# Optimization experiments

Hardware: AMD Instinct MI355X
Metric: run time of the kernel (lower is better)

## Reference

```python
import jax, jax.numpy as jnp
import numpy as np

ALPHA = 0.5      # APPNP teleport prob (AG_EAGCN alpha=0.5)
DEPTH = 3        # APPNP depth
PROP_NUMS = 3    # EAGCN propagation steps


def _adj_process(adj, eps):
    # adj[adj<eps]=0 ; symmetrize ; add I ; D^-1/2 A D^-1/2 (inf->0)
    N = adj.shape[1]
    adj = jnp.where(adj < eps, 0.0, adj)
    adj = 0.5 * (adj + jnp.swapaxes(adj, 1, 2))
    adj = adj + jnp.eye(N, dtype=adj.dtype)
    d = jnp.sum(adj, axis=2)                                   # [n, N]
    dinv = jnp.where(d > 0, 1.0 / jnp.sqrt(jnp.where(d > 0, d, 1.0)), 0.0)
    return adj * dinv[:, :, None] * dinv[:, None, :]


def _eagcn(seg, edge, ws1, bs1, ws11, bs11, ws2, bs2, ws3, bs3, wmlp, bmlp, wgcn, bgcn):
    n, c, h, w = seg.shape
    hw = h * w
    num_s = ws1.shape[0]
    # conv_s1 (1x1)
    seg_s = jnp.einsum('nchw,sc->nshw', seg, ws1) + bs1[None, :, None, None]
    theta_T = seg_s.reshape(n, num_s, hw)       # raw view, as in torch
    theta = seg_s.reshape(n, hw, num_s)         # raw view (NOT transpose)
    # channel attention: diag_channel_att = ca ca^T is rank-1 ->
    # theta @ (ca ca^T) @ theta_T = (theta@ca) outer (ca@theta_T)
    pooled = seg.mean(axis=(2, 3))                              # [n, c]
    ca = jax.nn.relu(pooled @ wmlp.T + bmlp)                    # [n, num_s]
    u = jnp.einsum('nps,ns->np', theta, ca)                     # [n, hw]
    v = jnp.einsum('ns,nsq->nq', ca, theta_T)                   # [n, hw]
    sim_c = _adj_process(u[:, :, None] * v[:, None, :], 0.15)
    # spatial branch
    seg_c = jnp.einsum('nchw,sc->nshw', seg, ws11) + bs11[None, :, None, None]
    sigma = seg_c.reshape(n, num_s, hw)
    sigma_T = seg_c.reshape(n, hw, num_s)
    sigma_out = jnp.einsum('nps,nsq->npq', sigma_T, sigma)      # [n, hw, hw]
    edge_m = seg * edge
    seg_ss = (ws2 * seg.max(axis=1) + bs2).reshape(n, 1, hw)    # 1x1 conv on 1 chan
    edge_mm = (ws3 * edge_m.max(axis=1) + bs3).reshape(n, hw, 1)
    sim_s = _adj_process(sigma_out * (edge_mm * seg_ss), 0.15)
    sim = _adj_process(sim_c + sim_s, 0.0)
    # GCN_layer: relu(conv1d(seg @ sim)) + seg, residual
    seg2 = seg.reshape(n, c, hw)
    seg_sim = jnp.einsum('nck,nkq->ncq', seg2, sim)
    out = jax.nn.relu(jnp.einsum('oc,ncq->noq', wgcn, seg_sim) + bgcn[None, :, None]) + seg2
    return out.reshape(n, c, h, w), sim


def _appnp(seg, adj, wa1, ba1, wa2, ba2):
    n, c, h, w = seg.shape
    x = seg.reshape(n, h * w, c)                                # raw view
    t = jax.nn.relu(jax.nn.relu(x @ wa1.T + ba1) @ wa2.T + ba2)
    out = t
    for _ in range(DEPTH):
        out = (1.0 - ALPHA) * jnp.einsum('npq,nqc->npc', adj, out) + ALPHA * t
    return out


def _forward(seg, edge, ws1, bs1, ws11, bs11, ws2, bs2, ws3, bs3,
             wmlp, bmlp, wgcn, bgcn, wa1, ba1, wa2, ba2):
    ori = seg
    n, c, h, w = seg.shape
    adjs = []
    for _ in range(PROP_NUMS):
        seg, adj = _eagcn(seg, edge, ws1, bs1, ws11, bs11, ws2, bs2, ws3, bs3,
                          wmlp, bmlp, wgcn, bgcn)
        adjs.append(adj)
    adj = (adjs[0] + adjs[1] + adjs[2]) / float(PROP_NUMS)      # mean aggregation
    adj = _adj_process(adj, 0.0)
    # graph regularizer
    dirichlet = jnp.einsum('nii->', adj)                        # sum of traces
    N = adj.shape[1]
    gamma = 0.1; beta = 0.1; alpha_r = 0.1
    rowsum = jnp.sum(adj, axis=2)                               # adj @ ones
    f_A = (-beta * jnp.sum(jnp.log(rowsum), axis=1)[:, None, None] / N
           + gamma * jnp.sqrt(jnp.sum(adj * adj)) / (N ** 2))
    reg = alpha_r * dirichlet + f_A                             # [n,1,1]
    out = _appnp(ori, adj, wa1, ba1, wa2, ba2).reshape(n, c, h, w)
    return out, reg


def setup_inputs() -> dict:
    key = jax.random.key(0)
    ks = jax.random.split(key, 10)
    n, c, h, w = 8, 256, 32, 32
    num_s, hid = 64, 3

    def lin(k, out_f, in_f):
        lim = 1.0 / np.sqrt(in_f)
        return jax.random.uniform(k, (out_f, in_f), jnp.float32, -lim, lim)

    return dict(
        seg=jax.random.normal(ks[0], (n, c, h, w), jnp.float32),
        edge=jax.random.uniform(ks[1], (n, c, h, w), jnp.float32),
        ws1=lin(ks[2], num_s, c), bs1=jnp.zeros((num_s,), jnp.float32),
        ws11=lin(ks[3], num_s, c), bs11=jnp.zeros((num_s,), jnp.float32),
        ws2=jnp.asarray(0.7, jnp.float32), bs2=jnp.asarray(0.1, jnp.float32),
        ws3=jnp.asarray(0.6, jnp.float32), bs3=jnp.asarray(0.1, jnp.float32),
        wmlp=lin(ks[4], num_s, c), bmlp=jnp.zeros((num_s,), jnp.float32),
        wgcn=lin(ks[5], c, c), bgcn=jnp.zeros((c,), jnp.float32),
        wa1=lin(ks[6], hid, c), ba1=jnp.zeros((hid,), jnp.float32),
        wa2=lin(ks[7], c, hid), ba2=jnp.zeros((c,), jnp.float32),
    )


def reference(seg, edge, ws1, bs1, ws11, bs11, ws2, bs2, ws3, bs3,
              wmlp, bmlp, wgcn, bgcn, wa1, ba1, wa2, ba2):
    return _forward(seg, edge, ws1, bs1, ws11, bs11, ws2, bs2, ws3, bs3,
                    wmlp, bmlp, wgcn, bgcn, wa1, ba1, wa2, ba2)
```

## Files before the change

### kernel.cpp

```cpp
#include <hip/hip_runtime.h>
#include <math.h>

#define NB 8
#define C 256
#define HW 1024
#define NS 64

typedef unsigned short u16;
typedef __attribute__((ext_vector_type(8))) short bf16x8;
typedef __attribute__((ext_vector_type(4))) float f32x4;

__device__ __forceinline__ u16 f2bf(float x) {
    union { float f; unsigned u; } v; v.f = x;
    unsigned r = v.u + 0x7fffu + ((v.u >> 16) & 1u);
    return (u16)(r >> 16);
}
__device__ __forceinline__ float bf2f(u16 h) {
    union { unsigned u; float f; } v; v.u = ((unsigned)h) << 16; return v.f;
}
__device__ __forceinline__ void splitbf(float x, u16& h, u16& l) {
    h = f2bf(x);
    l = f2bf(x - bf2f(h));
}

__device__ __forceinline__ float blockReduceSum(float v, float* s4) {
    #pragma unroll
    for (int o = 32; o; o >>= 1) v += __shfl_down(v, o);
    __syncthreads();
    if ((threadIdx.x & 63) == 0) s4[threadIdx.x >> 6] = v;
    __syncthreads();
    return s4[0] + s4[1] + s4[2] + s4[3];
}

__global__ void k_prepw(const float* __restrict__ ws1, const float* __restrict__ bs1,
                        const float* __restrict__ ws11, const float* __restrict__ bs11,
                        float* __restrict__ WCAT, float* __restrict__ BCAT) {
    int tid = blockIdx.x * 256 + threadIdx.x;
    if (tid < 64 * C) {
        WCAT[tid] = ws1[tid];
        WCAT[64 * C + tid] = ws11[tid];
    }
    if (tid < 64) { BCAT[tid] = bs1[tid]; BCAT[64 + tid] = bs11[tid]; }
}

template<int R, int CIN>
__global__ void k_transp(const float* __restrict__ in, long long sIn,
                         float* __restrict__ outp, long long sOut) {
    int ti = blockIdx.x, tj = blockIdx.y, n = blockIdx.z, tid = threadIdx.x;
    int i0 = ti * 64, j0 = tj * 64;
    const float* ib = in + (size_t)n * sIn;
    float* ob = outp + (size_t)n * sOut;
    __shared__ float L[64][65];
    for (int idx = tid; idx < 4096; idx += 256) {
        int r = idx >> 6, c = idx & 63;
        L[r][c] = ib[(size_t)(i0 + r) * CIN + (j0 + c)];
    }
    __syncthreads();
    for (int idx = tid; idx < 4096; idx += 256) {
        int r = idx >> 6, c = idx & 63;
        ob[(size_t)(j0 + r) * R + (i0 + c)] = L[c][r];
    }
}

__global__ void k_pooled(const float* __restrict__ seg, float* __restrict__ pooled) {
    int c = blockIdx.x, n = blockIdx.y, tid = threadIdx.x;
    const float* row = seg + ((size_t)n * C + c) * HW;
    float acc = row[tid] + row[tid + 256] + row[tid + 512] + row[tid + 768];
    __shared__ float s4[4];
    float r = blockReduceSum(acc, s4);
    if (tid == 0) pooled[n * C + c] = r * (1.0f / HW);
}

__global__ void k_ca(const float* __restrict__ pooled, const float* __restrict__ wmlp,
                     const float* __restrict__ bmlp, float* __restrict__ ca) {
    int n = blockIdx.x, s = threadIdx.x;
    __shared__ float pl[C];
    for (int i = s; i < C; i += 64) pl[i] = pooled[n * C + i];
    __syncthreads();
    float acc = 0.f;
    for (int c = 0; c < C; ++c) acc += pl[c] * wmlp[s * C + c];
    float r = acc + bmlp[s];
    ca[n * NS + s] = r > 0.f ? r : 0.f;
}

__global__ void k_maxes(const float* __restrict__ seg, const float* __restrict__ edge,
                        float* __restrict__ smax, float* __restrict__ emax) {
    int pos = blockIdx.x * 256 + threadIdx.x;
    int n = blockIdx.y, ch = blockIdx.z;
    const float* sb = seg + (size_t)n * C * HW + (size_t)(ch * 32) * HW + pos;
    const float* eb = edge + (size_t)n * C * HW + (size_t)(ch * 32) * HW + pos;
    float ms = -3.402823466e38f, me = -3.402823466e38f;
    #pragma unroll 8
    for (int c = 0; c < 32; ++c) {
        float s = sb[(size_t)c * HW];
        ms = fmaxf(ms, s);
        me = fmaxf(me, s * eb[(size_t)c * HW]);
    }
    smax[((size_t)ch * NB + n) * HW + pos] = ms;
    emax[((size_t)ch * NB + n) * HW + pos] = me;
}

__global__ void k_maxfin(const float* __restrict__ smax, const float* __restrict__ emax,
                         const float* __restrict__ ws2, const float* __restrict__ bs2,
                         const float* __restrict__ ws3, const float* __restrict__ bs3,
                         float* __restrict__ segss, float* __restrict__ edgemm) {
    int pos = blockIdx.x * 256 + threadIdx.x;
    int n = blockIdx.y;
    float ms = -3.402823466e38f, me = -3.402823466e38f;
    #pragma unroll
    for (int ch = 0; ch < 8; ++ch) {
        ms = fmaxf(ms, smax[((size_t)ch * NB + n) * HW + pos]);
        me = fmaxf(me, emax[((size_t)ch * NB + n) * HW + pos]);
    }
    segss[n * HW + pos] = ws2[0] * ms + bs2[0];
    edgemm[n * HW + pos] = ws3[0] * me + bs3[0];
}

__global__ void k_uv(const float* __restrict__ segsc, const float* __restrict__ ca,
                     float* __restrict__ u, float* __restrict__ vv) {
    int pos = blockIdx.x * 256 + threadIdx.x;
    int n = blockIdx.y, role = blockIdx.z;
    const float* flat = segsc + (size_t)n * 128 * HW;
    __shared__ float cs[NS];
    if (threadIdx.x < NS) cs[threadIdx.x] = ca[n * NS + threadIdx.x];
    __syncthreads();
    if (role == 0) {
        const float* base = flat + (size_t)pos * NS;
        float acc = 0.f;
        #pragma unroll
        for (int s = 0; s < NS; ++s) acc += base[s] * cs[s];
        u[n * HW + pos] = acc;
    } else {
        float acc = 0.f;
        #pragma unroll
        for (int s = 0; s < NS; ++s) acc += cs[s] * flat[(size_t)s * HW + pos];
        vv[n * HW + pos] = acc;
    }
}

__global__ __launch_bounds__(256) void k_bbuild(
    const float* __restrict__ Aflat, long long sA,
    const float* __restrict__ CT,
    const float* __restrict__ em, const float* __restrict__ ss,
    float* __restrict__ B, float* __restrict__ dsum) {
    constexpr int LDK = 72;
    constexpr int TSZ = 64 * LDK;
    __shared__ __align__(16) u16 sm[4 * 2 * TSZ];
    int pi = blockIdx.x, n = blockIdx.y, tid = threadIdx.x;
    int i = 0, base = 0;
    while (pi >= base + (16 - i)) { base += 16 - i; ++i; }
    int j = i + (pi - base);
    int i0 = i * 64, j0 = j * 64;
    bool diag = (i == j);
    const float* An = Aflat + (size_t)n * sA;
    const float* Cn = CT + (size_t)n * NS * HW;
    const float* emn = em + n * HW;
    const float* ssn = ss + n * HW;
    float* Bn = B + (size_t)n * HW * HW;

    auto stage = [&](int t, const float* src, int r0) {
        u16* hi = sm + t * 2 * TSZ;
        u16* lo = hi + TSZ;
        #pragma unroll
        for (int p = 0; p < 2; ++p) {
            int e = (p * 256 + tid) * 8;
            int r = e >> 6, k0 = e & 63;
            const float* s = src + (size_t)(r0 + r) * 64 + k0;
            float4 w0 = *(const float4*)s;
            float4 w1 = *(const float4*)(s + 4);
            float xs[8] = {w0.x, w0.y, w0.z, w0.w, w1.x, w1.y, w1.z, w1.w};
            u16 h[8], l[8];
            #pragma unroll
            for (int q = 0; q < 8; ++q) splitbf(xs[q], h[q], l[q]);
            int b = r * LDK + k0;
            *(bf16x8*)(hi + b) = (bf16x8){(short)h[0], (short)h[1], (short)h[2], (short)h[3],
                                          (short)h[4], (short)h[5], (short)h[6], (short)h[7]};
            *(bf16x8*)(lo + b) = (bf16x8){(short)l[0], (short)l[1], (short)l[2], (short)l[3],
                                          (short)l[4], (short)l[5], (short)l[6], (short)l[7]};
        }
    };
    stage(0, An, i0);
    stage(2, Cn, i0);
    if (!diag) { stage(1, An, j0); stage(3, Cn, j0); }
    __syncthreads();

    int lane = tid & 63, wv = tid >> 6;
    int g = lane >> 4;
    f32x4 acc1[4], acc2[4];
    #pragma unroll
    for (int ni = 0; ni < 4; ++ni) {
        acc1[ni] = (f32x4){0.f, 0.f, 0.f, 0.f};
        acc2[ni] = (f32x4){0.f, 0.f, 0.f, 0.f};
    }

    const u16* AiH = sm + 0 * 2 * TSZ; const u16* AiL = AiH + TSZ;
    const u16* AjH = sm + 1 * 2 * TSZ; const u16* AjL = AjH + TSZ;
    const u16* BiH = sm + 2 * 2 * TSZ; const u16* BiL = BiH + TSZ;
    const u16* BjH = sm + 3 * 2 * TSZ; const u16* BjL = BjH + TSZ;

    #pragma unroll
    for (int kk = 0; kk < 2; ++kk) {
        int kl = kk * 32 + g * 8;
        int arow = wv * 16 + (lane & 15);
        bf16x8 a1h = *(const bf16x8*)(AiH + arow * LDK + kl);
        bf16x8 a1l = *(const bf16x8*)(AiL + arow * LDK + kl);
        bf16x8 a2h, a2l;
        if (!diag) {
            a2h = *(const bf16x8*)(AjH + arow * LDK + kl);
            a2l = *(const bf16x8*)(AjL + arow * LDK + kl);
        }
        #pragma unroll
        for (int ni = 0; ni < 4; ++ni) {
            int brow = ni * 16 + (lane & 15);
            if (diag) {
                bf16x8 bh = *(const bf16x8*)(BiH + brow * LDK + kl);
                bf16x8 bl = *(const bf16x8*)(BiL + brow * LDK + kl);
                acc1[ni] = __builtin_amdgcn_mfma_f32_16x16x32_bf16(a1h, bh, acc1[ni], 0, 0, 0);
                acc1[ni] = __builtin_amdgcn_mfma_f32_16x16x32_bf16(a1h, bl, acc1[ni], 0, 0, 0);
                acc1[ni] = __builtin_amdgcn_mfma_f32_16x16x32_bf16(a1l, bh, acc1[ni], 0, 0, 0);
            } else {
                bf16x8 b1h = *(const bf16x8*)(BjH + brow * LDK + kl);
                bf16x8 b1l = *(const bf16x8*)(BjL + brow * LDK + kl);
                acc1[ni] = __builtin_amdgcn_mfma_f32_16x16x32_bf16(a1h, b1h, acc1[ni], 0, 0, 0);
                acc1[ni] = __builtin_amdgcn_mfma_f32_16x16x32_bf16(a1h, b1l, acc1[ni], 0, 0, 0);
                acc1[ni] = __builtin_amdgcn_mfma_f32_16x16x32_bf16(a1l, b1h, acc1[ni], 0, 0, 0);
                bf16x8 b2h = *(const bf16x8*)(BiH + brow * LDK + kl);
                bf16x8 b2l = *(const bf16x8*)(BiL + brow * LDK + kl);
                acc2[ni] = __builtin_amdgcn_mfma_f32_16x16x32_bf16(a2h, b2h, acc2[ni], 0, 0, 0);
                acc2[ni] = __builtin_amdgcn_mfma_f32_16x16x32_bf16(a2h, b2l, acc2[ni], 0, 0, 0);
                acc2[ni] = __builtin_amdgcn_mfma_f32_16x16x32_bf16(a2l, b2h, acc2[ni], 0, 0, 0);
            }
        }
    }
    __syncthreads();

    float* t1 = (float*)sm;
    float* t2 = t1 + 64 * 65;
    float x[4][4], y[4][4];
    #pragma unroll
    for (int ni = 0; ni < 4; ++ni) {
        int col = ni * 16 + (lane & 15);
        #pragma unroll
        for (int r = 0; r < 4; ++r) {
            int row = wv * 16 + g * 4 + r;
            float v1 = acc1[ni][r] * emn[i0 + row] * ssn[j0 + col];
            v1 = v1 < 0.15f ? 0.f : v1;
            x[ni][r] = v1;
            t1[row * 65 + col] = v1;
            if (!diag) {
                float v2 = acc2[ni][r] * emn[j0 + row] * ssn[i0 + col];
                v2 = v2 < 0.15f ? 0.f : v2;
                y[ni][r] = v2;
                t2[row * 65 + col] = v2;
            }
        }
    }
    __syncthreads();

    float rs1[4] = {0.f, 0.f, 0.f, 0.f}, rs2[4] = {0.f, 0.f, 0.f, 0.f};
    #pragma unroll
    for (int ni = 0; ni < 4; ++ni) {
        int col = ni * 16 + (lane & 15);
        #pragma unroll
        for (int r = 0; r < 4; ++r) {
            int row = wv * 16 + g * 4 + r;
            float s1 = 0.5f * (x[ni][r] + (diag ? t1[col * 65 + row] : t2[col * 65 + row]));
            Bn[(size_t)(i0 + row) * HW + j0 + col] = s1;
            rs1[r] += s1;
            if (!diag) {
                float s2 = 0.5f * (y[ni][r] + t1[col * 65 + row]);
                Bn[(size_t)(j0 + row) * HW + i0 + col] = s2;
                rs2[r] += s2;
            }
        }
    }
    #pragma unroll
    for (int r = 0; r < 4; ++r) {
        #pragma unroll
        for (int m = 1; m < 16; m <<= 1) {
            rs1[r] += __shfl_xor(rs1[r], m);
            rs2[r] += __shfl_xor(rs2[r], m);
        }
    }
    if ((lane & 15) == 0) {
        #pragma unroll
        for (int r = 0; r < 4; ++r) {
            int row = wv * 16 + g * 4 + r;
            atomicAdd(&dsum[n * HW + i0 + row], rs1[r]);
            if (!diag) atomicAdd(&dsum[n * HW + j0 + row], rs2[r]);
        }
    }
}

template<int BM, int BN, int MODE>
__global__ __launch_bounds__(256) void k_mfma2(
    const float* __restrict__ Af, long long sA, int lda,
    const float* __restrict__ Bf, long long sB, int ldb,
    int K,
    float* __restrict__ Cf, long long sCf, int ldc,
    const float* __restrict__ e1,
    const float* __restrict__ e2, long long se2) {
    constexpr int WM = BM / 32;
    constexpr int WN = BN / 32;
    constexpr int LDK = 72;
    __shared__ __align__(16) u16 sAH[BM * LDK], sAL[BM * LDK];
    __shared__ __align__(16) u16 sBH[BN * LDK], sBL[BN * LDK];
    int n = blockIdx.z;
    int q0 = blockIdx.x * BN, m0 = blockIdx.y * BM;
    int tid = threadIdx.x, lane = tid & 63, wv = tid >> 6;
    int wm = wv >> 1, wn = wv & 1;

    f32x4 acc[WM][WN];
    #pragma unroll
    for (int mi = 0; mi < WM; ++mi)
        #pragma unroll
        for (int ni = 0; ni < WN; ++ni)
            acc[mi][ni] = (f32x4){0.f, 0.f, 0.f, 0.f};

    for (int kt = 0; kt < K; kt += 64) {
        #pragma unroll
        for (int p = 0; p < BM / 32; ++p) {
            int e = (p * 256 + tid) * 8;
            int r = e >> 6, k0 = e & 63;
            const float* src = Af + (size_t)n * sA + (size_t)(m0 + r) * lda + kt + k0;
            float4 w0 = *(const float4*)src;
            float4 w1 = *(const float4*)(src + 4);
            float xs[8] = {w0.x, w0.y, w0.z, w0.w, w1.x, w1.y, w1.z, w1.w};
            u16 h[8], l[8];
            #pragma unroll
            for (int q = 0; q < 8; ++q) splitbf(xs[q], h[q], l[q]);
            int b = r * LDK + k0;
            *(bf16x8*)(sAH + b) = (bf16x8){(short)h[0], (short)h[1], (short)h[2], (short)h[3],
                                           (short)h[4], (short)h[5], (short)h[6], (short)h[7]};
            *(bf16x8*)(sAL + b) = (bf16x8){(short)l[0], (short)l[1], (short)l[2], (short)l[3],
                                           (short)l[4], (short)l[5], (short)l[6], (short)l[7]};
        }
        #pragma unroll
        for (int p = 0; p < BN / 32; ++p) {
            int e = (p * 256 + tid) * 8;
            int c = e >> 6, k0 = e & 63;
            const float* src = Bf + (size_t)n * sB + (size_t)(q0 + c) * ldb + kt + k0;
            float4 w0 = *(const float4*)src;
            float4 w1 = *(const float4*)(src + 4);
            float xs[8] = {w0.x, w0.y, w0.z, w0.w, w1.x, w1.y, w1.z, w1.w};
            u16 h[8], l[8];
            #pragma unroll
            for (int q = 0; q < 8; ++q) splitbf(xs[q], h[q], l[q]);
            int b = c * LDK + k0;
            *(bf16x8*)(sBH + b) = (bf16x8){(short)h[0], (short)h[1], (short)h[2], (short)h[3],
                                           (short)h[4], (short)h[5], (short)h[6], (short)h[7]};
            *(bf16x8*)(sBL + b) = (bf16x8){(short)l[0], (short)l[1], (short)l[2], (short)l[3],
                                           (short)l[4], (short)l[5], (short)l[6], (short)l[7]};
        }
        __syncthreads();
        #pragma unroll
        for (int kk = 0; kk < 2; ++kk) {
            int klocal = kk * 32 + (lane >> 4) * 8;
            bf16x8 aH[WM], aL[WM], bH[WN], bL[WN];
            #pragma unroll
            for (int mi = 0; mi < WM; ++mi) {
                int row = (wm * WM + mi) * 16 + (lane & 15);
                aH[mi] = *(const bf16x8*)(sAH + row * LDK + klocal);
                aL[mi] = *(const bf16x8*)(sAL + row * LDK + klocal);
            }
            #pragma unroll
            for (int ni = 0; ni < WN; ++ni) {
                int col = (wn * WN + ni) * 16 + (lane & 15);
                bH[ni] = *(const bf16x8*)(sBH + col * LDK + klocal);
                bL[ni] = *(const bf16x8*)(sBL + col * LDK + klocal);
            }
            #pragma unroll
            for (int mi = 0; mi < WM; ++mi)
                #pragma unroll
                for (int ni = 0; ni < WN; ++ni) {
                    acc[mi][ni] = __builtin_amdgcn_mfma_f32_16x16x32_bf16(aH[mi], bH[ni], acc[mi][ni], 0, 0, 0);
                    acc[mi][ni] = __builtin_amdgcn_mfma_f32_16x16x32_bf16(aH[mi], bL[ni], acc[mi][ni], 0, 0, 0);
                    acc[mi][ni] = __builtin_amdgcn_mfma_f32_16x16x32_bf16(aL[mi], bH[ni], acc[mi][ni], 0, 0, 0);
                }
        }
        __syncthreads();
    }

    #pragma unroll
    for (int mi = 0; mi < WM; ++mi) {
        #pragma unroll
        for (int ni = 0; ni < WN; ++ni) {
            int col = q0 + (wn * WN + ni) * 16 + (lane & 15);
            int rowb = m0 + (wm * WM + mi) * 16 + (lane >> 4) * 4;
            #pragma unroll
            for (int r = 0; r < 4; ++r) {
                int row = rowb + r;
                float val = acc[mi][ni][r];
                if (MODE == 0) {
                    Cf[(size_t)n * sCf + (size_t)col * ldc + row] = val;
                } else if (MODE == 2) {
                    val = fmaxf(val + e1[row], 0.f) + e2[(size_t)n * se2 + (size_t)row * ldc + col];
                    Cf[(size_t)n * sCf + (size_t)row * ldc + col] = val;
                } else if (MODE == 3) {
                    val = 0.5f * val + 0.5f * e2[(size_t)n * se2 + (size_t)row * ldc + col];
                    Cf[(size_t)n * sCf + (size_t)row * ldc + col] = val;
                } else if (MODE == 4) {
                    val = 0.5f * val + 0.5f * e2[(size_t)n * se2 + (size_t)row * HW + col];
                    Cf[(size_t)n * sCf + (size_t)col * ldc + row] = val;
                } else {
                    val = val + e1[row];
                    Cf[(size_t)n * sCf + (size_t)row * ldc + col] = val;
                }
            }
        }
    }
}

__global__ void k_dinv(const float* __restrict__ u, const float* __restrict__ vv,
                       const float* __restrict__ dsum,
                       float* __restrict__ dcinv, float* __restrict__ dsinv) {
    int p = blockIdx.x, n = blockIdx.y, tid = threadIdx.x;
    const float* un = u + n * HW;
    const float* vn = vv + n * HW;
    float up = un[p], vp = vn[p];
    float acc_c = 0.f;
    for (int q = tid; q < HW; q += 256) {
        float x = up * vn[q]; x = x < 0.15f ? 0.f : x;
        float y = un[q] * vp; y = y < 0.15f ? 0.f : y;
        acc_c += 0.5f * (x + y);
    }
    __shared__ float s4[4];
    acc_c = blockReduceSum(acc_c, s4);
    if (tid == 0) {
        dcinv[n * HW + p] = 1.0f / sqrtf(acc_c + 1.0f);
        dsinv[n * HW + p] = 1.0f / sqrtf(dsum[n * HW + p] + 1.0f);
    }
}

__global__ void k_simsum(const float* __restrict__ B, const float* __restrict__ u,
                         const float* __restrict__ vv, const float* __restrict__ dcinv,
                         const float* __restrict__ dsinv, float* __restrict__ dfinv) {
    int p = blockIdx.x, n = blockIdx.y, tid = threadIdx.x;
    const float* Bb = B + (size_t)n * HW * HW + (size_t)p * HW;
    const float* un = u + n * HW;
    const float* vn = vv + n * HW;
    const float* dci = dcinv + n * HW;
    const float* dsi = dsinv + n * HW;
    float up = un[p], vp = vn[p], dcp = dci[p], dsp = dsi[p];
    float acc = 0.f;
    for (int q = tid; q < HW; q += 256) {
        float x = up * vn[q]; x = x < 0.15f ? 0.f : x;
        float y = un[q] * vp; y = y < 0.15f ? 0.f : y;
        float delta = (q == p) ? 1.0f : 0.0f;
        float val = (0.5f * (x + y) + delta) * dcp * dci[q] + (Bb[q] + delta) * dsp * dsi[q];
        acc += val;
    }
    __shared__ float s4[4];
    acc = blockReduceSum(acc, s4);
    if (tid == 0) dfinv[n * HW + p] = 1.0f / sqrtf(acc + 1.0f);
}

__global__ void k_norm_accum(float* __restrict__ B, const float* __restrict__ u,
                             const float* __restrict__ vv, const float* __restrict__ dcinv,
                             const float* __restrict__ dsinv, const float* __restrict__ dfinv,
                             float* __restrict__ ACC, int first) {
    int p = blockIdx.x, n = blockIdx.y, tid = threadIdx.x;
    float* Bb = B + (size_t)n * HW * HW + (size_t)p * HW;
    float* Ab = ACC + (size_t)n * HW * HW + (size_t)p * HW;
    const float* un = u + n * HW;
    const float* vn = vv + n * HW;
    const float* dci = dcinv + n * HW;
    const float* dsi = dsinv + n * HW;
    const float* df = dfinv + n * HW;
    float up = un[p], vp = vn[p], dcp = dci[p], dsp = dsi[p], dfp = df[p];
    for (int q = tid; q < HW; q += 256) {
        float x = up * vn[q]; x = x < 0.15f ? 0.f : x;
        float y = un[q] * vp; y = y < 0.15f ? 0.f : y;
        float delta = (q == p) ? 1.0f : 0.0f;
        float sim_pre = (0.5f * (x + y) + delta) * dcp * dci[q] + (Bb[q] + delta) * dsp * dsi[q];
        float val = (sim_pre + delta) * dfp * df[q];
        Bb[q] = val;
        Ab[q] = first ? val : (Ab[q] + val);
    }
}

__global__ void k_final_rowsum(const float* __restrict__ ACC, float* __restrict__ dinv) {
    int p = blockIdx.x, n = blockIdx.y, tid = threadIdx.x;
    const float* Ab = ACC + (size_t)n * HW * HW + (size_t)p * HW;
    float acc = 0.f;
    for (int q = tid; q < HW; q += 256) acc += Ab[q];
    __shared__ float s4[4];
    acc = blockReduceSum(acc, s4);
    if (tid == 0) dinv[n * HW + p] = 1.0f / sqrtf(acc * (1.0f / 3.0f) + 1.0f);
}

__global__ void k_final_norm(float* __restrict__ ACC, const float* __restrict__ dinv,
                             float* __restrict__ rowsf, float* __restrict__ diagrow,
                             float* __restrict__ sqrow) {
    int p = blockIdx.x, n = blockIdx.y, tid = threadIdx.x;
    float* Ab = ACC + (size_t)n * HW * HW + (size_t)p * HW;
    const float* di = dinv + n * HW;
    float dp = di[p];
    float accr = 0.f, accsq = 0.f, accd = 0.f;
    for (int q = tid; q < HW; q += 256) {
        float val = (Ab[q] * (1.0f / 3.0f) + ((q == p) ? 1.f : 0.f)) * dp * di[q];
        Ab[q] = val;
        accr += val;
        accsq += val * val;
        if (q == p) accd = val;
    }
    __shared__ float s4[4];
    accr = blockReduceSum(accr, s4);
    accsq = blockReduceSum(accsq, s4);
    accd = blockReduceSum(accd, s4);
    if (tid == 0) {
        rowsf[n * HW + p] = accr;
        sqrow[n * HW + p] = accsq;
        diagrow[n * HW + p] = accd;
    }
}

__global__ void k_scal(const float* __restrict__ diagrow, const float* __restrict__ sqrow,
                       float* __restrict__ scal) {
    int tid = threadIdx.x;
    float a = 0.f, b = 0.f;
    for (int i = tid; i < NB * HW; i += 256) { a += diagrow[i]; b += sqrow[i]; }
    __shared__ float s4[4];
    a = blockReduceSum(a, s4);
    b = blockReduceSum(b, s4);
    if (tid == 0) { scal[0] = a; scal[1] = b; }
}

__global__ void k_reg(const float* __restrict__ rowsf, const float* __restrict__ scal,
                      float* __restrict__ outreg) {
    int n = blockIdx.x, tid = threadIdx.x;
    float acc = 0.f;
    for (int p = tid; p < HW; p += 256) acc += logf(rowsf[n * HW + p]);
    __shared__ float s4[4];
    acc = blockReduceSum(acc, s4);
    if (tid == 0) {
        float f = -0.1f * acc / 1024.0f + 0.1f * sqrtf(scal[1]) / 1048576.0f;
        outreg[n] = 0.1f * scal[0] + f;
    }
}

__global__ void k_appnp_t(const float* __restrict__ ori, const float* __restrict__ wa1,
                          const float* __restrict__ ba1, const float* __restrict__ wa2,
                          const float* __restrict__ ba2, float* __restrict__ T) {
    int p = blockIdx.x, n = blockIdx.y, tid = threadIdx.x;
    const float* x = ori + (size_t)n * C * HW + (size_t)p * C;
    float xv = x[tid];
    __shared__ float s4[4];
    __shared__ float h[3];
    float d0 = blockReduceSum(xv * wa1[0 * C + tid], s4);
    float d1 = blockReduceSum(xv * wa1[1 * C + tid], s4);
    float d2 = blockReduceSum(xv * wa1[2 * C + tid], s4);
    if (tid == 0) {
        h[0] = fmaxf(d0 + ba1[0], 0.f);
        h[1] = fmaxf(d1 + ba1[1], 0.f);
        h[2] = fmaxf(d2 + ba1[2], 0.f);
    }
    __syncthreads();
    float t = h[0] * wa2[tid * 3 + 0] + h[1] * wa2[tid * 3 + 1] + h[2] * wa2[tid * 3 + 2] + ba2[tid];
    T[(size_t)n * HW * C + (size_t)p * C + tid] = fmaxf(t, 0.f);
}

extern "C" void kernel_launch(void* const* d_in, const int* in_sizes, int n_in,
                              void* d_out, int out_size, void* d_ws, size_t ws_size,
                              hipStream_t stream) {
    const float* seg_in = (const float*)d_in[0];
    const float* edge   = (const float*)d_in[1];
    const float* ws1    = (const float*)d_in[2];
    const float* bs1    = (const float*)d_in[3];
    const float* ws11   = (const float*)d_in[4];
    const float* bs11   = (const float*)d_in[5];
    const float* ws2    = (const float*)d_in[6];
    const float* bs2    = (const float*)d_in[7];
    const float* ws3    = (const float*)d_in[8];
    const float* bs3    = (const float*)d_in[9];
    const float* wmlp   = (const float*)d_in[10];
    const float* bmlp   = (const float*)d_in[11];
    const float* wgcn   = (const float*)d_in[12];
    const float* bgcn   = (const float*)d_in[13];
    const float* wa1    = (const float*)d_in[14];
    const float* ba1    = (const float*)d_in[15];
    const float* wa2    = (const float*)d_in[16];
    const float* ba2    = (const float*)d_in[17];

    float* out = (float*)d_out;
    float* w = (float*)d_ws;
    float* SEG_A   = w; w += (size_t)NB * C * HW;
    float* SEG_SIMT= w; w += (size_t)NB * C * HW;
    float* SEGSC   = w; w += (size_t)NB * 128 * HW;
    float* SEGCT   = w; w += (size_t)NB * NS * HW;
    float* SEGT    = w; w += (size_t)NB * HW * C;
    float* TBUF    = w; w += (size_t)NB * HW * C;
    float* OBUF    = w; w += (size_t)NB * HW * C;
    float* BBUF    = w; w += (size_t)NB * HW * HW;
    float* ACCUM   = w; w += (size_t)NB * HW * HW;
    float* MAXS    = w; w += (size_t)8 * NB * HW;
    float* MAXE    = w; w += (size_t)8 * NB * HW;
    float* WCAT    = w; w += (size_t)128 * C;
    float* BCAT    = w; w += 128;
    float* ubuf    = w; w += NB * HW;
    float* vbuf    = w; w += NB * HW;
    float* ssbuf   = w; w += NB * HW;
    float* embuf   = w; w += NB * HW;
    float* dsum    = w; w += NB * HW;
    float* dcinv   = w; w += NB * HW;
    float* dsinv   = w; w += NB * HW;
    float* dfinv   = w; w += NB * HW;
    float* rowsf   = w; w += NB * HW;
    float* diagrow = w; w += NB * HW;
    float* sqrow   = w; w += NB * HW;
    float* pooled  = w; w += NB * C;
    float* cabuf   = w; w += NB * NS;
    float* scal    = w; w += 16;

    const long long sAdj = (long long)HW * HW;
    const long long sSeg = (long long)C * HW;
    const long long sSC  = (long long)128 * HW;

    k_prepw<<<dim3(64), 256, 0, stream>>>(ws1, bs1, ws11, bs11, WCAT, BCAT);

    for (int it = 0; it < 3; ++it) {
        const float* seg_src = (it == 0) ? seg_in : SEG_A;
        k_transp<C, HW><<<dim3(4, 16, NB), 256, 0, stream>>>(seg_src, sSeg, SEGT, sSeg);
        k_mfma2<64, 64, 5><<<dim3(16, 2, NB), 256, 0, stream>>>(
            WCAT, 0, C, SEGT, sSeg, C, C,
            SEGSC, sSC, HW, BCAT, nullptr, 0);
        k_transp<NS, HW><<<dim3(1, 16, NB), 256, 0, stream>>>(SEGSC + (size_t)64 * HW, sSC, SEGCT, (long long)NS * HW);
        k_pooled<<<dim3(C, NB), 256, 0, stream>>>(seg_src, pooled);
        k_ca<<<dim3(NB), 64, 0, stream>>>(pooled, wmlp, bmlp, cabuf);
        k_maxes<<<dim3(4, NB, 8), 256, 0, stream>>>(seg_src, edge, MAXS, MAXE);
        k_maxfin<<<dim3(4, NB), 256, 0, stream>>>(MAXS, MAXE, ws2, bs2, ws3, bs3, ssbuf, embuf);
        k_uv<<<dim3(4, NB, 2), 256, 0, stream>>>(SEGSC, cabuf, ubuf, vbuf);
        hipMemsetAsync(dsum, 0, (size_t)NB * HW * sizeof(float), stream);
        k_bbuild<<<dim3(136, NB), 256, 0, stream>>>(SEGSC + (size_t)64 * HW, sSC, SEGCT,
                                                    embuf, ssbuf, BBUF, dsum);
        k_dinv<<<dim3(HW, NB), 256, 0, stream>>>(ubuf, vbuf, dsum, dcinv, dsinv);
        k_simsum<<<dim3(HW, NB), 256, 0, stream>>>(BBUF, ubuf, vbuf, dcinv, dsinv, dfinv);
        k_norm_accum<<<dim3(HW, NB), 256, 0, stream>>>(BBUF, ubuf, vbuf, dcinv, dsinv, dfinv,
                                                       ACCUM, it == 0 ? 1 : 0);
        k_mfma2<64, 64, 0><<<dim3(16, 4, NB), 256, 0, stream>>>(
            seg_src, sSeg, HW, BBUF, sAdj, HW, HW,
            SEG_SIMT, sSeg, C, nullptr, nullptr, 0);
        k_mfma2<64, 64, 2><<<dim3(16, 4, NB), 256, 0, stream>>>(
            wgcn, 0, C, SEG_SIMT, sSeg, C, C,
            SEG_A, sSeg, HW, bgcn, seg_src, sSeg);
    }

    k_final_rowsum<<<dim3(HW, NB), 256, 0, stream>>>(ACCUM, dcinv);
    k_final_norm<<<dim3(HW, NB), 256, 0, stream>>>(ACCUM, dcinv, rowsf, diagrow, sqrow);
    k_scal<<<dim3(1), 256, 0, stream>>>(diagrow, sqrow, scal);
    k_reg<<<dim3(NB), 256, 0, stream>>>(rowsf, scal, out + (size_t)NB * C * HW);

    k_appnp_t<<<dim3(HW, NB), 256, 0, stream>>>(seg_in, wa1, ba1, wa2, ba2, TBUF);
    k_transp<HW, C><<<dim3(16, 4, NB), 256, 0, stream>>>(TBUF, sSeg, SEG_SIMT, sSeg);
    k_mfma2<64, 64, 3><<<dim3(16, 4, NB), 256, 0, stream>>>(
        SEG_SIMT, sSeg, HW, ACCUM, sAdj, HW, HW,
        TBUF, sSeg, HW, nullptr, SEG_SIMT, sSeg);
    k_mfma2<64, 64, 3><<<dim3(16, 4, NB), 256, 0, stream>>>(
        TBUF, sSeg, HW, ACCUM, sAdj, HW, HW,
        OBUF, sSeg, HW, nullptr, SEG_SIMT, sSeg);
    k_mfma2<64, 64, 4><<<dim3(16, 4, NB), 256, 0, stream>>>(
        OBUF, sSeg, HW, ACCUM, sAdj, HW, HW,
        out, sSeg, C, nullptr, SEG_SIMT, sSeg);
}
```

Baseline: 701.4 us.

## Store operands pre-split into bf16 hi/lo planes instead of splitting in GEMM loads

Producers now write every GEMM operand as separate bf16 hi and lo arrays: transposes, epilogues, the normalization kernels and the weights. The MFMA and bbuild kernels then copy bf16x8 vectors straight into shared memory without per-element float splitting. This removes the repeated split work inside the GEMM tile loops. Operand reads drop from 4 to 4 bytes total (hi+lo), so traffic is the same, but the large HW×HW matrices are re-read many times. It adds extra write traffic wherever both fp32 and split copies are kept, and it grows the workspace.

```diff
diff --git a/kernel.cpp b/kernel.cpp
--- a/kernel.cpp
+++ b/kernel.cpp
@@ -32,24 +32,33 @@
     return s4[0] + s4[1] + s4[2] + s4[3];
 }
 
+__global__ void k_presplit(const float* __restrict__ in, u16* __restrict__ oh,
+                           u16* __restrict__ ol, int nElem) {
+    for (int i = blockIdx.x * 256 + threadIdx.x; i < nElem; i += gridDim.x * 256) {
+        u16 h, l; splitbf(in[i], h, l);
+        oh[i] = h; ol[i] = l;
+    }
+}
+
 __global__ void k_prepw(const float* __restrict__ ws1, const float* __restrict__ bs1,
                         const float* __restrict__ ws11, const float* __restrict__ bs11,
-                        float* __restrict__ WCAT, float* __restrict__ BCAT) {
+                        u16* __restrict__ WCH, u16* __restrict__ WCL, float* __restrict__ BCAT) {
     int tid = blockIdx.x * 256 + threadIdx.x;
     if (tid < 64 * C) {
-        WCAT[tid] = ws1[tid];
-        WCAT[64 * C + tid] = ws11[tid];
+        u16 h, l;
+        splitbf(ws1[tid], h, l);  WCH[tid] = h;          WCL[tid] = l;
+        splitbf(ws11[tid], h, l); WCH[64 * C + tid] = h; WCL[64 * C + tid] = l;
     }
     if (tid < 64) { BCAT[tid] = bs1[tid]; BCAT[64 + tid] = bs11[tid]; }
 }
 
-template<int R, int CIN>
-__global__ void k_transp(const float* __restrict__ in, long long sIn,
-                         float* __restrict__ outp, long long sOut) {
+template<int R, int CIN, bool WF32>
+__global__ void k_transp_split(const float* __restrict__ in, long long sIn,
+                               u16* __restrict__ oh, u16* __restrict__ ol,
+                               float* __restrict__ of, long long sOut) {
     int ti = blockIdx.x, tj = blockIdx.y, n = blockIdx.z, tid = threadIdx.x;
     int i0 = ti * 64, j0 = tj * 64;
     const float* ib = in + (size_t)n * sIn;
-    float* ob = outp + (size_t)n * sOut;
     __shared__ float L[64][65];
     for (int idx = tid; idx < 4096; idx += 256) {
         int r = idx >> 6, c = idx & 63;
@@ -58,7 +67,11 @@
     __syncthreads();
     for (int idx = tid; idx < 4096; idx += 256) {
         int r = idx >> 6, c = idx & 63;
-        ob[(size_t)(j0 + r) * R + (i0 + c)] = L[c][r];
+        size_t o = (size_t)n * sOut + (size_t)(j0 + r) * R + (i0 + c);
+        float val = L[c][r];
+        u16 h, l; splitbf(val, h, l);
+        oh[o] = h; ol[o] = l;
+        if (WF32) of[o] = val;
     }
 }
 
@@ -139,8 +152,8 @@
 }
 
 __global__ __launch_bounds__(256) void k_bbuild(
-    const float* __restrict__ Aflat, long long sA,
-    const float* __restrict__ CT,
+    const u16* __restrict__ AH, const u16* __restrict__ AL, long long sA,
+    const u16* __restrict__ CTH, const u16* __restrict__ CTL, long long sCT,
     const float* __restrict__ em, const float* __restrict__ ss,
     float* __restrict__ B, float* __restrict__ dsum) {
     constexpr int LDK = 72;
@@ -152,36 +165,30 @@
     int j = i + (pi - base);
     int i0 = i * 64, j0 = j * 64;
     bool diag = (i == j);
-    const float* An = Aflat + (size_t)n * sA;
-    const float* Cn = CT + (size_t)n * NS * HW;
+    const u16* AnH = AH + (size_t)n * sA;
+    const u16* AnL = AL + (size_t)n * sA;
+    const u16* CnH = CTH + (size_t)n * sCT;
+    const u16* CnL = CTL + (size_t)n * sCT;
     const float* emn = em + n * HW;
     const float* ssn = ss + n * HW;
     float* Bn = B + (size_t)n * HW * HW;
 
-    auto stage = [&](int t, const float* src, int r0) {
+    auto stage = [&](int t, const u16* srcH, const u16* srcL, int r0) {
         u16* hi = sm + t * 2 * TSZ;
         u16* lo = hi + TSZ;
         #pragma unroll
         for (int p = 0; p < 2; ++p) {
             int e = (p * 256 + tid) * 8;
             int r = e >> 6, k0 = e & 63;
-            const float* s = src + (size_t)(r0 + r) * 64 + k0;
-            float4 w0 = *(const float4*)s;
-            float4 w1 = *(const float4*)(s + 4);
-            float xs[8] = {w0.x, w0.y, w0.z, w0.w, w1.x, w1.y, w1.z, w1.w};
-            u16 h[8], l[8];
-            #pragma unroll
-            for (int q = 0; q < 8; ++q) splitbf(xs[q], h[q], l[q]);
+            size_t off = (size_t)(r0 + r) * 64 + k0;
             int b = r * LDK + k0;
-            *(bf16x8*)(hi + b) = (bf16x8){(short)h[0], (short)h[1], (short)h[2], (short)h[3],
-                                          (short)h[4], (short)h[5], (short)h[6], (short)h[7]};
-            *(bf16x8*)(lo + b) = (bf16x8){(short)l[0], (short)l[1], (short)l[2], (short)l[3],
-                                          (short)l[4], (short)l[5], (short)l[6], (short)l[7]};
+            *(bf16x8*)(hi + b) = *(const bf16x8*)(srcH + off);
+            *(bf16x8*)(lo + b) = *(const bf16x8*)(srcL + off);
         }
     };
-    stage(0, An, i0);
-    stage(2, Cn, i0);
-    if (!diag) { stage(1, An, j0); stage(3, Cn, j0); }
+    stage(0, AnH, AnL, i0);
+    stage(2, CnH, CnL, i0);
+    if (!diag) { stage(1, AnH, AnL, j0); stage(3, CnH, CnL, j0); }
     __syncthreads();
 
     int lane = tid & 63, wv = tid >> 6;
@@ -293,11 +300,12 @@
 }
 
 template<int BM, int BN, int MODE>
-__global__ __launch_bounds__(256) void k_mfma2(
-    const float* __restrict__ Af, long long sA, int lda,
-    const float* __restrict__ Bf, long long sB, int ldb,
+__global__ __launch_bounds__(256) void k_mfma3(
+    const u16* __restrict__ AH, const u16* __restrict__ AL, long long sA, int lda,
+    const u16* __restrict__ BH, const u16* __restrict__ BL, long long sB, int ldb,
     int K,
-    float* __restrict__ Cf, long long sCf, int ldc,
+    float* __restrict__ Cf, u16* __restrict__ CH, u16* __restrict__ CL,
+    long long sC, int ldc,
     const float* __restrict__ e1,
     const float* __restrict__ e2, long long se2) {
     constexpr int WM = BM / 32;
@@ -322,35 +330,19 @@
         for (int p = 0; p < BM / 32; ++p) {
             int e = (p * 256 + tid) * 8;
             int r = e >> 6, k0 = e & 63;
-            const float* src = Af + (size_t)n * sA + (size_t)(m0 + r) * lda + kt + k0;
-            float4 w0 = *(const float4*)src;
-            float4 w1 = *(const float4*)(src + 4);
-            float xs[8] = {w0.x, w0.y, w0.z, w0.w, w1.x, w1.y, w1.z, w1.w};
-            u16 h[8], l[8];
-            #pragma unroll
-            for (int q = 0; q < 8; ++q) splitbf(xs[q], h[q], l[q]);
+            size_t off = (size_t)n * sA + (size_t)(m0 + r) * lda + kt + k0;
             int b = r * LDK + k0;
-            *(bf16x8*)(sAH + b) = (bf16x8){(short)h[0], (short)h[1], (short)h[2], (short)h[3],
-                                           (short)h[4], (short)h[5], (short)h[6], (short)h[7]};
-            *(bf16x8*)(sAL + b) = (bf16x8){(short)l[0], (short)l[1], (short)l[2], (short)l[3],
-                                           (short)l[4], (short)l[5], (short)l[6], (short)l[7]};
+            *(bf16x8*)(sAH + b) = *(const bf16x8*)(AH + off);
+            *(bf16x8*)(sAL + b) = *(const bf16x8*)(AL + off);
         }
         #pragma unroll
         for (int p = 0; p < BN / 32; ++p) {
             int e = (p * 256 + tid) * 8;
             int c = e >> 6, k0 = e & 63;
-            const float* src = Bf + (size_t)n * sB + (size_t)(q0 + c) * ldb + kt + k0;
-            float4 w0 = *(const float4*)src;
-            float4 w1 = *(const float4*)(src + 4);
-            float xs[8] = {w0.x, w0.y, w0.z, w0.w, w1.x, w1.y, w1.z, w1.w};
-            u16 h[8], l[8];
-            #pragma unroll
-            for (int q = 0; q < 8; ++q) splitbf(xs[q], h[q], l[q]);
+            size_t off = (size_t)n * sB + (size_t)(q0 + c) * ldb + kt + k0;
             int b = c * LDK + k0;
-            *(bf16x8*)(sBH + b) = (bf16x8){(short)h[0], (short)h[1], (short)h[2], (short)h[3],
-                                           (short)h[4], (short)h[5], (short)h[6], (short)h[7]};
-            *(bf16x8*)(sBL + b) = (bf16x8){(short)l[0], (short)l[1], (short)l[2], (short)l[3],
-                                           (short)l[4], (short)l[5], (short)l[6], (short)l[7]};
+            *(bf16x8*)(sBH + b) = *(const bf16x8*)(BH + off);
+            *(bf16x8*)(sBL + b) = *(const bf16x8*)(BL + off);
         }
         __syncthreads();
         #pragma unroll
@@ -392,19 +384,29 @@
                 int row = rowb + r;
                 float val = acc[mi][ni][r];
                 if (MODE == 0) {
-                    Cf[(size_t)n * sCf + (size_t)col * ldc + row] = val;
+                    u16 h, l; splitbf(val, h, l);
+                    size_t o = (size_t)n * sC + (size_t)col * ldc + row;
+                    CH[o] = h; CL[o] = l;
                 } else if (MODE == 2) {
                     val = fmaxf(val + e1[row], 0.f) + e2[(size_t)n * se2 + (size_t)row * ldc + col];
-                    Cf[(size_t)n * sCf + (size_t)row * ldc + col] = val;
+                    size_t o = (size_t)n * sC + (size_t)row * ldc + col;
+                    Cf[o] = val;
+                    u16 h, l; splitbf(val, h, l);
+                    CH[o] = h; CL[o] = l;
                 } else if (MODE == 3) {
                     val = 0.5f * val + 0.5f * e2[(size_t)n * se2 + (size_t)row * ldc + col];
-                    Cf[(size_t)n * sCf + (size_t)row * ldc + col] = val;
+                    size_t o = (size_t)n * sC + (size_t)row * ldc + col;
+                    u16 h, l; splitbf(val, h, l);
+                    CH[o] = h; CL[o] = l;
                 } else if (MODE == 4) {
                     val = 0.5f * val + 0.5f * e2[(size_t)n * se2 + (size_t)row * HW + col];
-                    Cf[(size_t)n * sCf + (size_t)col * ldc + row] = val;
+                    Cf[(size_t)n * sC + (size_t)col * ldc + row] = val;
                 } else {
                     val = val + e1[row];
-                    Cf[(size_t)n * sCf + (size_t)row * ldc + col] = val;
+                    size_t o = (size_t)n * sC + (size_t)row * ldc + col;
+                    Cf[o] = val;
+                    u16 h, l; splitbf(val, h, l);
+                    CH[o] = h; CL[o] = l;
                 }
             }
         }
@@ -455,12 +457,15 @@
     if (tid == 0) dfinv[n * HW + p] = 1.0f / sqrtf(acc + 1.0f);
 }
 
-__global__ void k_norm_accum(float* __restrict__ B, const float* __restrict__ u,
+__global__ void k_norm_accum(const float* __restrict__ B, const float* __restrict__ u,
                              const float* __restrict__ vv, const float* __restrict__ dcinv,
                              const float* __restrict__ dsinv, const float* __restrict__ dfinv,
+                             u16* __restrict__ SMH, u16* __restrict__ SML,
                              float* __restrict__ ACC, int first) {
     int p = blockIdx.x, n = blockIdx.y, tid = threadIdx.x;
-    float* Bb = B + (size_t)n * HW * HW + (size_t)p * HW;
+    const float* Bb = B + (size_t)n * HW * HW + (size_t)p * HW;
+    u16* Sh = SMH + (size_t)n * HW * HW + (size_t)p * HW;
+    u16* Sl = SML + (size_t)n * HW * HW + (size_t)p * HW;
     float* Ab = ACC + (size_t)n * HW * HW + (size_t)p * HW;
     const float* un = u + n * HW;
     const float* vn = vv + n * HW;
@@ -474,7 +479,8 @@
         float delta = (q == p) ? 1.0f : 0.0f;
         float sim_pre = (0.5f * (x + y) + delta) * dcp * dci[q] + (Bb[q] + delta) * dsp * dsi[q];
         float val = (sim_pre + delta) * dfp * df[q];
-        Bb[q] = val;
+        u16 h, l; splitbf(val, h, l);
+        Sh[q] = h; Sl[q] = l;
         Ab[q] = first ? val : (Ab[q] + val);
     }
 }
@@ -489,17 +495,21 @@
     if (tid == 0) dinv[n * HW + p] = 1.0f / sqrtf(acc * (1.0f / 3.0f) + 1.0f);
 }
 
-__global__ void k_final_norm(float* __restrict__ ACC, const float* __restrict__ dinv,
+__global__ void k_final_norm(const float* __restrict__ ACC, const float* __restrict__ dinv,
+                             u16* __restrict__ ADJH, u16* __restrict__ ADJL,
                              float* __restrict__ rowsf, float* __restrict__ diagrow,
                              float* __restrict__ sqrow) {
     int p = blockIdx.x, n = blockIdx.y, tid = threadIdx.x;
-    float* Ab = ACC + (size_t)n * HW * HW + (size_t)p * HW;
+    const float* Ab = ACC + (size_t)n * HW * HW + (size_t)p * HW;
+    u16* Oh = ADJH + (size_t)n * HW * HW + (size_t)p * HW;
+    u16* Ol = ADJL + (size_t)n * HW * HW + (size_t)p * HW;
     const float* di = dinv + n * HW;
     float dp = di[p];
     float accr = 0.f, accsq = 0.f, accd = 0.f;
     for (int q = tid; q < HW; q += 256) {
         float val = (Ab[q] * (1.0f / 3.0f) + ((q == p) ? 1.f : 0.f)) * dp * di[q];
-        Ab[q] = val;
+        u16 h, l; splitbf(val, h, l);
+        Oh[q] = h; Ol[q] = l;
         accr += val;
         accsq += val * val;
         if (q == p) accd = val;
@@ -583,82 +593,104 @@
     const float* ba2    = (const float*)d_in[17];
 
     float* out = (float*)d_out;
-    float* w = (float*)d_ws;
-    float* SEG_A   = w; w += (size_t)NB * C * HW;
-    float* SEG_SIMT= w; w += (size_t)NB * C * HW;
-    float* SEGSC   = w; w += (size_t)NB * 128 * HW;
-    float* SEGCT   = w; w += (size_t)NB * NS * HW;
-    float* SEGT    = w; w += (size_t)NB * HW * C;
-    float* TBUF    = w; w += (size_t)NB * HW * C;
-    float* OBUF    = w; w += (size_t)NB * HW * C;
-    float* BBUF    = w; w += (size_t)NB * HW * HW;
-    float* ACCUM   = w; w += (size_t)NB * HW * HW;
-    float* MAXS    = w; w += (size_t)8 * NB * HW;
-    float* MAXE    = w; w += (size_t)8 * NB * HW;
-    float* WCAT    = w; w += (size_t)128 * C;
-    float* BCAT    = w; w += 128;
-    float* ubuf    = w; w += NB * HW;
-    float* vbuf    = w; w += NB * HW;
-    float* ssbuf   = w; w += NB * HW;
-    float* embuf   = w; w += NB * HW;
-    float* dsum    = w; w += NB * HW;
-    float* dcinv   = w; w += NB * HW;
-    float* dsinv   = w; w += NB * HW;
-    float* dfinv   = w; w += NB * HW;
-    float* rowsf   = w; w += NB * HW;
-    float* diagrow = w; w += NB * HW;
-    float* sqrow   = w; w += NB * HW;
-    float* pooled  = w; w += NB * C;
-    float* cabuf   = w; w += NB * NS;
-    float* scal    = w; w += 16;
+    char* wb = (char*)d_ws;
+    size_t off = 0;
+    auto nf = [&](size_t elems) -> float* {
+        float* p = (float*)(wb + off); off += ((elems * 4 + 255) & ~(size_t)255); return p; };
+    auto nu = [&](size_t elems) -> u16* {
+        u16* p = (u16*)(wb + off); off += ((elems * 2 + 255) & ~(size_t)255); return p; };
+
+    float* SEG_A   = nf((size_t)NB * C * HW);
+    float* SEGSC   = nf((size_t)NB * 128 * HW);
+    float* TT      = nf((size_t)NB * C * HW);
+    float* TBUF    = nf((size_t)NB * HW * C);
+    float* BBUF    = nf((size_t)NB * HW * HW);
+    float* ACCUM   = nf((size_t)NB * HW * HW);
+    float* MAXS    = nf((size_t)8 * NB * HW);
+    float* MAXE    = nf((size_t)8 * NB * HW);
+    float* BCAT    = nf(128);
+    float* ubuf    = nf(NB * HW);
+    float* vbuf    = nf(NB * HW);
+    float* ssbuf   = nf(NB * HW);
+    float* embuf   = nf(NB * HW);
+    float* dsum    = nf(NB * HW);
+    float* dcinv   = nf(NB * HW);
+    float* dsinv   = nf(NB * HW);
+    float* dfinv   = nf(NB * HW);
+    float* rowsf   = nf(NB * HW);
+    float* diagrow = nf(NB * HW);
+    float* sqrow   = nf(NB * HW);
+    float* pooled  = nf(NB * C);
+    float* cabuf   = nf(NB * NS);
+    float* scal    = nf(16);
+    u16* SAH  = nu((size_t)NB * C * HW);   u16* SAL  = nu((size_t)NB * C * HW);
+    u16* TGH  = nu((size_t)NB * HW * C);   u16* TGL  = nu((size_t)NB * HW * C);
+    u16* WCH  = nu((size_t)128 * C);       u16* WCL  = nu((size_t)128 * C);
+    u16* WGH  = nu((size_t)C * C);         u16* WGL  = nu((size_t)C * C);
+    u16* SCH  = nu((size_t)NB * 128 * HW); u16* SCL  = nu((size_t)NB * 128 * HW);
+    u16* CTH  = nu((size_t)NB * HW * NS);  u16* CTL  = nu((size_t)NB * HW * NS);
+    u16* SMH  = nu((size_t)NB * HW * HW);  u16* SML  = nu((size_t)NB * HW * HW);
+    u16* SIMTH= nu((size_t)NB * HW * C);   u16* SIMTL= nu((size_t)NB * HW * C);
+    u16* TTH  = nu((size_t)NB * C * HW);   u16* TTL  = nu((size_t)NB * C * HW);
+    u16* X1H  = nu((size_t)NB * C * HW);   u16* X1L  = nu((size_t)NB * C * HW);
+    u16* X2H  = nu((size_t)NB * C * HW);   u16* X2L  = nu((size_t)NB * C * HW);
+    u16* ADJH = SMH;
+    u16* ADJL = SML;
 
     const long long sAdj = (long long)HW * HW;
     const long long sSeg = (long long)C * HW;
     const long long sSC  = (long long)128 * HW;
-
-    k_prepw<<<dim3(64), 256, 0, stream>>>(ws1, bs1, ws11, bs11, WCAT, BCAT);
+    const long long sCT  = (long long)HW * NS;
+
+    k_prepw<<<dim3(64), 256, 0, stream>>>(ws1, bs1, ws11, bs11, WCH, WCL, BCAT);
+    k_presplit<<<dim3(64), 256, 0, stream>>>(wgcn, WGH, WGL, C * C);
+    k_presplit<<<dim3(2048), 256, 0, stream>>>(seg_in, SAH, SAL, NB * C * HW);
 
     for (int it = 0; it < 3; ++it) {
         const float* seg_src = (it == 0) ? seg_in : SEG_A;
-        k_transp<C, HW><<<dim3(4, 16, NB), 256, 0, stream>>>(seg_src, sSeg, SEGT, sSeg);
-        k_mfma2<64, 64, 5><<<dim3(16, 2, NB), 256, 0, stream>>>(
-            WCAT, 0, C, SEGT, sSeg, C, C,
-            SEGSC, sSC, HW, BCAT, nullptr, 0);
-        k_transp<NS, HW><<<dim3(1, 16, NB), 256, 0, stream>>>(SEGSC + (size_t)64 * HW, sSC, SEGCT, (long long)NS * HW);
+        k_transp_split<C, HW, false><<<dim3(4, 16, NB), 256, 0, stream>>>(
+            seg_src, sSeg, TGH, TGL, nullptr, sSeg);
+        k_mfma3<64, 64, 5><<<dim3(16, 2, NB), 256, 0, stream>>>(
+            WCH, WCL, 0, C, TGH, TGL, sSeg, C, C,
+            SEGSC, SCH, SCL, sSC, HW, BCAT, nullptr, 0);
+        k_transp_split<NS, HW, false><<<dim3(1, 16, NB), 256, 0, stream>>>(
+            SEGSC + (size_t)64 * HW, sSC, CTH, CTL, nullptr, sCT);
         k_pooled<<<dim3(C, NB), 256, 0, stream>>>(seg_src, pooled);
         k_ca<<<dim3(NB), 64, 0, stream>>>(pooled, wmlp, bmlp, cabuf);
         k_maxes<<<dim3(4, NB, 8), 256, 0, stream>>>(seg_src, edge, MAXS, MAXE);
         k_maxfin<<<dim3(4, NB), 256, 0, stream>>>(MAXS, MAXE, ws2, bs2, ws3, bs3, ssbuf, embuf);
         k_uv<<<dim3(4, NB, 2), 256, 0, stream>>>(SEGSC, cabuf, ubuf, vbuf);
         hipMemsetAsync(dsum, 0, (size_t)NB * HW * sizeof(float), stream);
-        k_bbuild<<<dim3(136, NB), 256, 0, stream>>>(SEGSC + (size_t)64 * HW, sSC, SEGCT,
-                                                    embuf, ssbuf, BBUF, dsum);
+        k_bbuild<<<dim3(136, NB), 256, 0, stream>>>(
+            SCH + (size_t)64 * HW, SCL + (size_t)64 * HW, sSC,
+            CTH, CTL, sCT, embuf, ssbuf, BBUF, dsum);
         k_dinv<<<dim3(HW, NB), 256, 0, stream>>>(ubuf, vbuf, dsum, dcinv, dsinv);
         k_simsum<<<dim3(HW, NB), 256, 0, stream>>>(BBUF, ubuf, vbuf, dcinv, dsinv, dfinv);
         k_norm_accum<<<dim3(HW, NB), 256, 0, stream>>>(BBUF, ubuf, vbuf, dcinv, dsinv, dfinv,
-                                                       ACCUM, it == 0 ? 1 : 0);
-        k_mfma2<64, 64, 0><<<dim3(16, 4, NB), 256, 0, stream>>>(
-            seg_src, sSeg, HW, BBUF, sAdj, HW, HW,
-            SEG_SIMT, sSeg, C, nullptr, nullptr, 0);
-        k_mfma2<64, 64, 2><<<dim3(16, 4, NB), 256, 0, stream>>>(
-            wgcn, 0, C, SEG_SIMT, sSeg, C, C,
-            SEG_A, sSeg, HW, bgcn, seg_src, sSeg);
+                                                       SMH, SML, ACCUM, it == 0 ? 1 : 0);
+        k_mfma3<64, 64, 0><<<dim3(16, 4, NB), 256, 0, stream>>>(
+            SAH, SAL, sSeg, HW, SMH, SML, sAdj, HW, HW,
+            nullptr, SIMTH, SIMTL, sSeg, C, nullptr, nullptr, 0);
+        k_mfma3<64, 64, 2><<<dim3(16, 4, NB), 256, 0, stream>>>(
+            WGH, WGL, 0, C, SIMTH, SIMTL, sSeg, C, C,
+            SEG_A, SAH, SAL, sSeg, HW, bgcn, seg_src, sSeg);
     }
 
     k_final_rowsum<<<dim3(HW, NB), 256, 0, stream>>>(ACCUM, dcinv);
-    k_final_norm<<<dim3(HW, NB), 256, 0, stream>>>(ACCUM, dcinv, rowsf, diagrow, sqrow);
+    k_final_norm<<<dim3(HW, NB), 256, 0, stream>>>(ACCUM, dcinv, ADJH, ADJL, rowsf, diagrow, sqrow);
     k_scal<<<dim3(1), 256, 0, stream>>>(diagrow, sqrow, scal);
     k_reg<<<dim3(NB), 256, 0, stream>>>(rowsf, scal, out + (size_t)NB * C * HW);
 
     k_appnp_t<<<dim3(HW, NB), 256, 0, stream>>>(seg_in, wa1, ba1, wa2, ba2, TBUF);
-    k_transp<HW, C><<<dim3(16, 4, NB), 256, 0, stream>>>(TBUF, sSeg, SEG_SIMT, sSeg);
-    k_mfma2<64, 64, 3><<<dim3(16, 4, NB), 256, 0, stream>>>(
-        SEG_SIMT, sSeg, HW, ACCUM, sAdj, HW, HW,
-        TBUF, sSeg, HW, nullptr, SEG_SIMT, sSeg);
-    k_mfma2<64, 64, 3><<<dim3(16, 4, NB), 256, 0, stream>>>(
-        TBUF, sSeg, HW, ACCUM, sAdj, HW, HW,
-        OBUF, sSeg, HW, nullptr, SEG_SIMT, sSeg);
-    k_mfma2<64, 64, 4><<<dim3(16, 4, NB), 256, 0, stream>>>(
-        OBUF, sSeg, HW, ACCUM, sAdj, HW, HW,
-        out, sSeg, C, nullptr, SEG_SIMT, sSeg);
-}
+    k_transp_split<HW, C, true><<<dim3(16, 4, NB), 256, 0, stream>>>(
+        TBUF, sSeg, TTH, TTL, TT, sSeg);
+    k_mfma3<64, 64, 3><<<dim3(16, 4, NB), 256, 0, stream>>>(
+        TTH, TTL, sSeg, HW, ADJH, ADJL, sAdj, HW, HW,
+        nullptr, X1H, X1L, sSeg, HW, nullptr, TT, sSeg);
+    k_mfma3<64, 64, 3><<<dim3(16, 4, NB), 256, 0, stream>>>(
+        X1H, X1L, sSeg, HW, ADJH, ADJL, sAdj, HW, HW,
+        nullptr, X2H, X2L, sSeg, HW, nullptr, TT, sSeg);
+    k_mfma3<64, 64, 4><<<dim3(16, 4, NB), 256, 0, stream>>>(
+        X2H, X2L, sSeg, HW, ADJH, ADJL, sAdj, HW, HW,
+        out, nullptr, nullptr, sSeg, C, nullptr, TT, sSeg);
+}
```

After: 583.9 us. 1.2x faster.
